# Kernel tuning notes

Hardware: AMD Instinct MI355X
Metric: run time of the kernel (lower is better)

## Reference

```python
import jax, jax.numpy as jnp
import numpy as np

B, C, H, W, HEADS = 8, 192, 128, 128, 4
EPS = 1e-5  # nn.LayerNorm default eps


def conv_block(x, pw_w, pw_b, dw_w, dw_b):
    # pointwise 1x1 conv (C->C) followed by depthwise 3x3 conv (Restormer-style convBlock)
    x = jnp.einsum('bchw,oc->bohw', x, pw_w) + pw_b[None, :, None, None]
    x = jax.lax.conv_general_dilated(
        x, dw_w, window_strides=(1, 1), padding='SAME',
        dimension_numbers=('NCHW', 'OIHW', 'NCHW'),
        feature_group_count=x.shape[1]) + dw_b[None, :, None, None]
    return x


def setup_inputs() -> dict:
    key = jax.random.key(0)
    ks = jax.random.split(key, 10)
    def n(k, shape, scale=0.02):
        return jax.random.normal(k, shape, jnp.float32) * scale
    return {
        'x': jax.random.normal(ks[0], (B, C, H, W), jnp.float32),
        'ln_w': jnp.ones((C,), jnp.float32),
        'ln_b': jnp.zeros((C,), jnp.float32),
        'q_pw_w': n(ks[1], (C, C)), 'q_pw_b': jnp.zeros((C,), jnp.float32),
        'q_dw_w': n(ks[2], (C, 1, 3, 3)), 'q_dw_b': jnp.zeros((C,), jnp.float32),
        'k_pw_w': n(ks[3], (C, C)), 'k_pw_b': jnp.zeros((C,), jnp.float32),
        'k_dw_w': n(ks[4], (C, 1, 3, 3)), 'k_dw_b': jnp.zeros((C,), jnp.float32),
        'v_pw_w': n(ks[5], (C, C)), 'v_pw_b': jnp.zeros((C,), jnp.float32),
        'v_dw_w': n(ks[6], (C, 1, 3, 3)), 'v_dw_b': jnp.zeros((C,), jnp.float32),
        'f_w': n(ks[7], (C, C)), 'f_b': jnp.zeros((C,), jnp.float32),
        'alpha': jnp.ones((), jnp.float32),
    }


def reference(x, ln_w, ln_b, q_pw_w, q_pw_b, q_dw_w, q_dw_b,
              k_pw_w, k_pw_b, k_dw_w, k_dw_b,
              v_pw_w, v_pw_b, v_dw_w, v_dw_b, f_w, f_b, alpha):
    b, c, h, w = x.shape
    s = c // HEADS
    # LayerNorm over channel axis (x.transpose(1,3) -> LN(last dim=C) -> transpose back)
    xt = jnp.transpose(x, (0, 3, 2, 1))  # (B,W,H,C)
    mu = jnp.mean(xt, axis=-1, keepdims=True)
    var = jnp.var(xt, axis=-1, keepdims=True)
    xt = (xt - mu) * jax.lax.rsqrt(var + EPS) * ln_w + ln_b
    xn = jnp.transpose(xt, (0, 3, 2, 1))  # (B,C,H,W) - normalized; residual uses this

    def flat(t):
        # NCHW -> (B, W*H, C), W-major flatten as in the torch code (transpose(1,3) then reshape)
        return jnp.transpose(t, (0, 3, 2, 1)).reshape(b, w * h, c)

    Q = flat(conv_block(xn, q_pw_w, q_pw_b, q_dw_w, q_dw_b))
    K = flat(conv_block(xn, k_pw_w, k_pw_b, k_dw_w, k_dw_b))
    V = flat(conv_block(xn, v_pw_w, v_pw_b, v_dw_w, v_dw_b))

    def heads(t):
        return jnp.transpose(t.reshape(b, w * h, HEADS, s), (0, 2, 1, 3))  # (B,heads,t,s)

    Qh, Kh, Vh = heads(Q), heads(K), heads(V)
    # channel-wise cross-covariance attention: (s x s) per head, learnable temperature alpha
    att = jax.nn.softmax(jnp.einsum('bhts,bhtq->bhsq', Kh, Qh) / alpha, axis=-1)
    out = jnp.einsum('bhts,bhsq->bhtq', Vh, att)  # (B,heads,t,s)
    # view(b,heads,t,s).transpose(2,3).reshape(b, C, H, W) exactly as in torch
    out = jnp.transpose(out, (0, 1, 3, 2)).reshape(b, c, h, w)
    y = jnp.einsum('bchw,oc->bohw', out, f_w) + f_b[None, :, None, None] + xn
    return y
```

## Files before the change

### kernel.cpp

```cpp
#include <hip/hip_runtime.h>
#include <hip/hip_bf16.h>

#define B_    8
#define C_    192
#define H_    128
#define W_    128
#define HW_   16384
#define HEADS 4
#define S_    48
#define EPS_  1e-5f

typedef __hip_bfloat16 bf16;
typedef unsigned short u16;
typedef __attribute__((ext_vector_type(8))) short short8;
typedef __attribute__((ext_vector_type(4))) short short4v;
typedef __attribute__((ext_vector_type(4))) float f32x4;
typedef __attribute__((ext_vector_type(8))) u16 u16x8;
typedef __attribute__((ext_vector_type(4))) u16 u16x4;
typedef __attribute__((ext_vector_type(2))) u16 u16x2;

__device__ inline float ld(const bf16* p)  { return __bfloat162float(*p); }
__device__ inline void  st(float* p, float v) { *p = v; }
__device__ inline void  st(bf16* p, float v)  { *p = __float2bfloat16(v); }
__device__ inline float b2f(u16 u) {
  unsigned v = (unsigned)u << 16;
  return __builtin_bit_cast(float, v);
}
__device__ inline u16 f2b(float f) {
  return __builtin_bit_cast(u16, __float2bfloat16(f));
}

__global__ __launch_bounds__(256) void zero_kernel(float* p, int n) {
  int i = blockIdx.x * 256 + threadIdx.x;
  if (i < n) p[i] = 0.f;
}

__global__ __launch_bounds__(256) void ln_kernel(
    const float* __restrict__ x, const float* __restrict__ lw,
    const float* __restrict__ lb, bf16* __restrict__ xn) {
  __shared__ float4 sS[8][32];
  __shared__ float4 sQ[8][32];
  int tid = threadIdx.x;
  int g = tid >> 5, q = tid & 31;
  int blk = blockIdx.x;
  int b = blk >> 7;
  int pos = (blk & 127) * 128 + q * 4;
  const float* xp = x + (size_t)b * C_ * HW_ + pos;

  float4 v[24];
  float s0 = 0.f, s1 = 0.f, s2 = 0.f, s3 = 0.f;
  float q0 = 0.f, q1 = 0.f, q2 = 0.f, q3 = 0.f;
#pragma unroll
  for (int cc = 0; cc < 24; cc++) {
    int c = g * 24 + cc;
    v[cc] = *(const float4*)&xp[(size_t)c * HW_];
    s0 += v[cc].x; s1 += v[cc].y; s2 += v[cc].z; s3 += v[cc].w;
    q0 += v[cc].x * v[cc].x; q1 += v[cc].y * v[cc].y;
    q2 += v[cc].z * v[cc].z; q3 += v[cc].w * v[cc].w;
  }
  sS[g][q] = make_float4(s0, s1, s2, s3);
  sQ[g][q] = make_float4(q0, q1, q2, q3);
  __syncthreads();

  float S[4] = {}, Qs[4] = {};
#pragma unroll
  for (int gg = 0; gg < 8; gg++) {
    float4 a = sS[gg][q];
    float4 bq = sQ[gg][q];
    S[0] += a.x;  S[1] += a.y;  S[2] += a.z;  S[3] += a.w;
    Qs[0] += bq.x; Qs[1] += bq.y; Qs[2] += bq.z; Qs[3] += bq.w;
  }
  float mu[4], r[4];
#pragma unroll
  for (int i = 0; i < 4; i++) {
    mu[i] = S[i] * (1.0f / C_);
    r[i] = rsqrtf(Qs[i] * (1.0f / C_) - mu[i] * mu[i] + EPS_);
  }

  u16* op = (u16*)xn + (size_t)b * C_ * HW_ + pos;
#pragma unroll
  for (int cc = 0; cc < 24; cc++) {
    int c = g * 24 + cc;
    float wv = lw[c], bv = lb[c];
    u16x4 o;
    o.x = f2b((v[cc].x - mu[0]) * r[0] * wv + bv);
    o.y = f2b((v[cc].y - mu[1]) * r[1] * wv + bv);
    o.z = f2b((v[cc].z - mu[2]) * r[2] * wv + bv);
    o.w = f2b((v[cc].w - mu[3]) * r[3] * wv + bv);
    *(u16x4*)&op[(size_t)c * HW_] = o;
  }
}

#define SWR 200
template <bool RES, typename OutT>
__global__ __launch_bounds__(256) void pw_mfma_kernel(
    const bf16* __restrict__ in, const float* __restrict__ wt,
    const float* __restrict__ bias, const bf16* __restrict__ residual,
    OutT* __restrict__ out) {
  __shared__ __align__(16) u16 sW[64 * SWR];
  __shared__ __align__(16) u16 sX[32 * 256];
  int tid = threadIdx.x;
  int posBase = blockIdx.x * 256;
  int oBase = blockIdx.y * 64;
  int b = blockIdx.z;
  int wv = tid >> 6, lane = tid & 63;
  int quad = lane >> 4, l15 = lane & 15;

#pragma unroll
  for (int i = 0; i < 12; i++) {
    int u = (tid + i * 256) * 4;
    int r = u / 192, c = u % 192;
    float4 f = *(const float4*)&wt[(size_t)(oBase + r) * 192 + c];
    ushort4 hv;
    hv.x = f2b(f.x); hv.y = f2b(f.y); hv.z = f2b(f.z); hv.w = f2b(f.w);
    *(ushort4*)&sW[r * SWR + c] = hv;
  }

  int chl = tid >> 3;
  int oct0 = tid & 7;
  int swz = ((chl >> 3) & 3) << 1;
  const u16* xrow = (const u16*)in + ((size_t)b * C_ + chl) * HW_ + posBase;

  u16x8 vg[4];
#pragma unroll
  for (int i = 0; i < 4; i++)
    vg[i] = *(const u16x8*)&xrow[(oct0 + 8 * i) * 8];

  f32x4 acc[4][4] = {};

  for (int kc = 0; kc < 6; kc++) {
#pragma unroll
    for (int i = 0; i < 4; i++) {
      int s = (oct0 + 8 * i) ^ swz;
      *(u16x8*)&sX[chl * 256 + s * 8] = vg[i];
    }
    __syncthreads();

    if (kc < 5) {
#pragma unroll
      for (int i = 0; i < 4; i++)
        vg[i] = *(const u16x8*)&xrow[(size_t)(kc + 1) * 32 * HW_ + (oct0 + 8 * i) * 8];
    }

    short8 afrag[4];
#pragma unroll
    for (int mt = 0; mt < 4; mt++)
      afrag[mt] = *(const short8*)&sW[(mt * 16 + l15) * SWR + kc * 32 + quad * 8];
#pragma unroll
    for (int nt = 0; nt < 4; nt++) {
      int p = wv * 64 + nt * 16 + l15;
      int po = p >> 3, pr = p & 7;
      int sb = po ^ (quad << 1);
      const u16* bp = &sX[(quad * 8) * 256 + sb * 8 + pr];
      short8 bfrag;
#pragma unroll
      for (int j = 0; j < 8; j++)
        bfrag[j] = (short)bp[j * 256];
#pragma unroll
      for (int mt = 0; mt < 4; mt++)
        acc[mt][nt] = __builtin_amdgcn_mfma_f32_16x16x32_bf16(
            afrag[mt], bfrag, acc[mt][nt], 0, 0, 0);
    }
    __syncthreads();
  }

#pragma unroll
  for (int mt = 0; mt < 4; mt++) {
#pragma unroll
    for (int r = 0; r < 4; r++) {
      int o = oBase + mt * 16 + quad * 4 + r;
      float bs = bias[o];
      size_t rowoff = ((size_t)b * C_ + o) * HW_;
#pragma unroll
      for (int nt = 0; nt < 4; nt++) {
        int p = posBase + wv * 64 + nt * 16 + l15;
        float val = acc[mt][nt][r] + bs;
        if (RES) val += ld(residual + rowoff + p);
        st(out + rowoff + p, val);
      }
    }
  }
}

__global__ __launch_bounds__(256) void dw_kernel(
    const bf16* __restrict__ in, const float* __restrict__ w9,
    const float* __restrict__ bias, bf16* __restrict__ out) {
  __shared__ __align__(16) u16 sT[18 * 128];
  int blk = blockIdx.x;
  int bc = blk >> 3;
  int h0 = (blk & 7) * 16;
  int c = bc % C_;
  const u16* ip = (const u16*)in + (size_t)bc * HW_;
  int tid = threadIdx.x;

  for (int ch = tid; ch < 288; ch += 256) {
    int r = ch >> 4, g = ch & 15;
    int gh = h0 - 1 + r;
    u16x8 val = {};
    if (gh >= 0 && gh < H_) val = *(const u16x8*)&ip[gh * 128 + g * 8];
    *(u16x8*)&sT[r * 128 + g * 8] = val;
  }
  __syncthreads();

  int r_o = tid >> 4, g = tid & 15;
  const float* wp = w9 + c * 9;
  float acc[8];
#pragma unroll
  for (int j = 0; j < 8; j++) acc[j] = bias[c];
#pragma unroll
  for (int k = 0; k < 3; k++) {
    int rr = r_o + k;
    u16x8 mid = *(const u16x8*)&sT[rr * 128 + g * 8];
    float m[8];
#pragma unroll
    for (int j = 0; j < 8; j++) m[j] = b2f(mid[j]);
    float lv = g ? b2f(sT[rr * 128 + g * 8 - 1]) : 0.f;
    float rv = (g < 15) ? b2f(sT[rr * 128 + g * 8 + 8]) : 0.f;
    float wl = wp[k * 3], wc = wp[k * 3 + 1], wr = wp[k * 3 + 2];
#pragma unroll
    for (int j = 0; j < 8; j++) {
      float left  = (j == 0) ? lv : m[j - 1];
      float right = (j == 7) ? rv : m[j + 1];
      acc[j] += wl * left + wc * m[j] + wr * right;
    }
  }
  u16x8 o;
#pragma unroll
  for (int j = 0; j < 8; j++) o[j] = f2b(acc[j]);
  *(u16x8*)((u16*)out + (size_t)bc * HW_ + (h0 + r_o) * 128 + g * 8) = o;
}

__global__ __launch_bounds__(256) void dwt_kernel(
    const bf16* __restrict__ in, const float* __restrict__ w9,
    const float* __restrict__ bias, bf16* __restrict__ out) {
  __shared__ __align__(16) u16 sIn[130 * 32];
  int blk = blockIdx.x;
  int bc = blk >> 3;
  int w0 = (blk & 7) * 16;
  int c = bc % C_;
  const u16* ip = (const u16*)in + (size_t)bc * HW_;
  int tid = threadIdx.x;

  for (int idx = tid; idx < 520; idx += 256) {
    int r = idx >> 2, seg = idx & 3;
    int h = r - 1;
    int w = w0 - 8 + seg * 8;
    u16x8 val = {};
    if (h >= 0 && h < H_ && w >= 0 && w < W_)
      val = *(const u16x8*)&ip[h * W_ + w];
    int colp = (seg * 8) ^ (((r >> 3) & 3) << 4);
    *(u16x8*)&sIn[r * 32 + colp] = val;
  }
  __syncthreads();

  int wl = tid & 15, ho = tid >> 4;
  const float* wp = w9 + c * 9;
  float wk[9];
#pragma unroll
  for (int i = 0; i < 9; i++) wk[i] = wp[i];
  float bs = bias[c];
  float acc[8];
#pragma unroll
  for (int j = 0; j < 8; j++) acc[j] = bs;
#pragma unroll
  for (int k = 0; k < 10; k++) {
    int r = ho * 8 + k;
    int swz = ((r >> 3) & 3) << 4;
    float lv = b2f(sIn[r * 32 + ((wl + 7) ^ swz)]);
    float mv = b2f(sIn[r * 32 + ((wl + 8) ^ swz)]);
    float rv = b2f(sIn[r * 32 + ((wl + 9) ^ swz)]);
#pragma unroll
    for (int kh = 0; kh < 3; kh++) {
      int j = k - kh;
      if (j >= 0 && j < 8)
        acc[j] += wk[kh * 3] * lv + wk[kh * 3 + 1] * mv + wk[kh * 3 + 2] * rv;
    }
  }
  u16x8 o;
#pragma unroll
  for (int j = 0; j < 8; j++) o[j] = f2b(acc[j]);
  *(u16x8*)((u16*)out + (size_t)bc * HW_ + (w0 + wl) * H_ + ho * 8) = o;
}

__global__ __launch_bounds__(256) void gram_mfma_kernel(
    const bf16* __restrict__ Q, const bf16* __restrict__ K,
    float* __restrict__ logits) {
  __shared__ float sP[4][S_ * S_];
  int bh = blockIdx.y;
  int b = bh >> 2, hd = bh & 3;
  int tid = threadIdx.x;
  int wv = tid >> 6, lane = tid & 63;
  int quad = lane >> 4, l15 = lane & 15;
  const u16* Qb = (const u16*)Q + ((size_t)b * C_ + hd * S_) * HW_;
  const u16* Kb = (const u16*)K + ((size_t)b * C_ + hd * S_) * HW_;
  int pbase = blockIdx.x * 1024 + wv * 256 + quad * 8;

  f32x4 acc[3][3] = {};
#pragma unroll
  for (int t = 0; t < 8; t++) {
    int p = pbase + t * 32;
    short8 a[3], bb[3];
#pragma unroll
    for (int mi = 0; mi < 3; mi++)
      a[mi] = *(const short8*)&Kb[(size_t)(mi * 16 + l15) * HW_ + p];
#pragma unroll
    for (int ni = 0; ni < 3; ni++)
      bb[ni] = *(const short8*)&Qb[(size_t)(ni * 16 + l15) * HW_ + p];
#pragma unroll
    for (int mi = 0; mi < 3; mi++)
#pragma unroll
      for (int ni = 0; ni < 3; ni++)
        acc[mi][ni] = __builtin_amdgcn_mfma_f32_16x16x32_bf16(
            a[mi], bb[ni], acc[mi][ni], 0, 0, 0);
  }

#pragma unroll
  for (int mi = 0; mi < 3; mi++)
#pragma unroll
    for (int r = 0; r < 4; r++) {
      int sk = mi * 16 + quad * 4 + r;
#pragma unroll
      for (int ni = 0; ni < 3; ni++)
        sP[wv][sk * S_ + ni * 16 + l15] = acc[mi][ni][r];
    }
  __syncthreads();

  float* lp = logits + (size_t)bh * S_ * S_;
  for (int e = tid; e < S_ * S_; e += 256)
    atomicAdd(&lp[e], sP[0][e] + sP[1][e] + sP[2][e] + sP[3][e]);
}

__global__ __launch_bounds__(256) void softmax_kernel(
    const float* __restrict__ logits, const float* __restrict__ alpha,
    float* __restrict__ att) {
  int row = blockIdx.x * 256 + threadIdx.x;
  if (row >= B_ * HEADS * S_) return;
  float inv_a = 1.0f / alpha[0];
  const float* lp = logits + (size_t)row * S_;
  float v[S_];
  float m = -1e30f;
  for (int i = 0; i < S_; i++) {
    v[i] = lp[i] * inv_a;
    m = fmaxf(m, v[i]);
  }
  float s = 0.f;
  for (int i = 0; i < S_; i++) { v[i] = expf(v[i] - m); s += v[i]; }
  float inv_s = 1.0f / s;
  float* ap = att + (size_t)row * S_;
  for (int i = 0; i < S_; i++) ap[i] = v[i] * inv_s;
}

#define AVP 264
#define ATP 72
__global__ __launch_bounds__(256) void av_mfma_kernel(
    const bf16* __restrict__ V, const float* __restrict__ att,
    bf16* __restrict__ out) {
  __shared__ __align__(16) u16 sV[64 * AVP];
  __shared__ __align__(16) u16 sA[48 * ATP];
  int bh = blockIdx.y;
  int b = bh >> 2, hd = bh & 3;
  int p0 = blockIdx.x * 256;
  int tid = threadIdx.x;
  int wv = tid >> 6, lane = tid & 63;
  int quad = lane >> 4, l15 = lane & 15;
  const u16* Vb = (const u16*)V + ((size_t)b * C_ + hd * S_) * HW_ + p0;
  const float* ap = att + (size_t)bh * S_ * S_;

#pragma unroll
  for (int i = 0; i < 6; i++) {
    int e = tid + i * 256;
    int s = e >> 5, p8 = (e & 31) * 8;
    u16x8 v8 = *(const u16x8*)&Vb[(size_t)s * HW_ + p8];
    *(u16x8*)&sV[s * AVP + p8] = v8;
  }
  {
    unsigned* zp = (unsigned*)&sV[48 * AVP];
    for (int e = tid; e < 16 * AVP / 2; e += 256) zp[e] = 0;
  }
  for (int e = tid; e < S_ * S_; e += 256) {
    int q = e % S_, s = e / S_;
    sA[q * ATP + s] = f2b(ap[e]);
  }
  for (int e = tid; e < S_ * 16; e += 256) {
    int q = e >> 4, s = 48 + (e & 15);
    sA[q * ATP + s] = 0;
  }
  __syncthreads();

  f32x4 acc[3][4] = {};
#pragma unroll
  for (int kc = 0; kc < 2; kc++) {
    short8 afrag[3];
#pragma unroll
    for (int mt = 0; mt < 3; mt++)
      afrag[mt] = *(const short8*)&sA[(mt * 16 + l15) * ATP + kc * 32 + quad * 8];
#pragma unroll
    for (int nt = 0; nt < 4; nt++) {
      int p = wv * 64 + nt * 16 + l15;
      short8 bfrag;
#pragma unroll
      for (int j = 0; j < 8; j++)
        bfrag[j] = (short)sV[(kc * 32 + quad * 8 + j) * AVP + p];
#pragma unroll
      for (int mt = 0; mt < 3; mt++)
        acc[mt][nt] = __builtin_amdgcn_mfma_f32_16x16x32_bf16(
            afrag[mt], bfrag, acc[mt][nt], 0, 0, 0);
    }
  }

  bf16* ob = out + ((size_t)b * C_ + hd * S_) * HW_ + p0;
#pragma unroll
  for (int mt = 0; mt < 3; mt++)
#pragma unroll
    for (int r = 0; r < 4; r++) {
      int q = mt * 16 + quad * 4 + r;
#pragma unroll
      for (int nt = 0; nt < 4; nt++) {
        int p = wv * 64 + nt * 16 + l15;
        st(ob + (size_t)q * HW_ + p, acc[mt][nt][r]);
      }
    }
}

extern "C" void kernel_launch(void* const* d_in, const int* in_sizes, int n_in,
                              void* d_out, int out_size, void* d_ws, size_t ws_size,
                              hipStream_t stream) {
  const float* x      = (const float*)d_in[0];
  const float* ln_w   = (const float*)d_in[1];
  const float* ln_b   = (const float*)d_in[2];
  const float* q_pw_w = (const float*)d_in[3];
  const float* q_pw_b = (const float*)d_in[4];
  const float* q_dw_w = (const float*)d_in[5];
  const float* q_dw_b = (const float*)d_in[6];
  const float* k_pw_w = (const float*)d_in[7];
  const float* k_pw_b = (const float*)d_in[8];
  const float* k_dw_w = (const float*)d_in[9];
  const float* k_dw_b = (const float*)d_in[10];
  const float* v_pw_w = (const float*)d_in[11];
  const float* v_pw_b = (const float*)d_in[12];
  const float* v_dw_w = (const float*)d_in[13];
  const float* v_dw_b = (const float*)d_in[14];
  const float* f_w    = (const float*)d_in[15];
  const float* f_b    = (const float*)d_in[16];
  const float* alpha  = (const float*)d_in[17];
  float* out = (float*)d_out;

  size_t N = (size_t)B_ * C_ * HW_;
  bf16* xn   = (bf16*)d_ws;
  bf16* tmp  = xn + N;
  bf16* A    = tmp + N;
  float* logits = (float*)(A + N);
  float* att    = logits + (size_t)B_ * HEADS * S_ * S_;
  bf16* Kb     = (bf16*)d_out;

  int nlog = B_ * HEADS * S_ * S_;
  zero_kernel<<<dim3(nlog / 256), 256, 0, stream>>>(logits, nlog);

  ln_kernel<<<dim3(B_ * HW_ / 128), 256, 0, stream>>>(x, ln_w, ln_b, xn);

  dim3 gG(HW_ / 256, C_ / 64, B_);
  int dwBlocks = B_ * C_ * 8;

  pw_mfma_kernel<false, bf16><<<gG, 256, 0, stream>>>(xn, q_pw_w, q_pw_b, nullptr, tmp);
  dw_kernel<<<dwBlocks, 256, 0, stream>>>(tmp, q_dw_w, q_dw_b, A);
  pw_mfma_kernel<false, bf16><<<gG, 256, 0, stream>>>(xn, k_pw_w, k_pw_b, nullptr, tmp);
  dw_kernel<<<dwBlocks, 256, 0, stream>>>(tmp, k_dw_w, k_dw_b, Kb);
  gram_mfma_kernel<<<dim3(16, B_ * HEADS), 256, 0, stream>>>(A, Kb, logits);
  softmax_kernel<<<dim3(6), 256, 0, stream>>>(logits, alpha, att);
  pw_mfma_kernel<false, bf16><<<gG, 256, 0, stream>>>(xn, v_pw_w, v_pw_b, nullptr, tmp);
  dwt_kernel<<<dwBlocks, 256, 0, stream>>>(tmp, v_dw_w, v_dw_b, A);
  av_mfma_kernel<<<dim3(HW_ / 256, B_ * HEADS), 256, 0, stream>>>(A, att, tmp);
  pw_mfma_kernel<true, float><<<gG, 256, 0, stream>>>(tmp, f_w, f_b, xn, out);
}
```

Baseline: 458.5 us.

## Store LN and attention outputs in MFMA-fragment-tiled layout, drop LDS staging in pointwise GEMM

Result: faster. 447.3 us (-2.4%).

```diff
diff --git a/kernel.cpp b/kernel.cpp
--- a/kernel.cpp
+++ b/kernel.cpp
@@ -19,6 +19,7 @@
 typedef __attribute__((ext_vector_type(4))) u16 u16x4;
 typedef __attribute__((ext_vector_type(2))) u16 u16x2;
 
+
 __device__ inline float ld(const bf16* p)  { return __bfloat162float(*p); }
 __device__ inline void  st(float* p, float v) { *p = v; }
 __device__ inline void  st(bf16* p, float v)  { *p = __float2bfloat16(v); }
@@ -47,17 +48,19 @@
   int pos = (blk & 127) * 128 + q * 4;
   const float* xp = x + (size_t)b * C_ * HW_ + pos;
 
-  float4 v[24];
+  float4 v[3][8];
   float s0 = 0.f, s1 = 0.f, s2 = 0.f, s3 = 0.f;
   float q0 = 0.f, q1 = 0.f, q2 = 0.f, q3 = 0.f;
 #pragma unroll
-  for (int cc = 0; cc < 24; cc++) {
-    int c = g * 24 + cc;
-    v[cc] = *(const float4*)&xp[(size_t)c * HW_];
-    s0 += v[cc].x; s1 += v[cc].y; s2 += v[cc].z; s3 += v[cc].w;
-    q0 += v[cc].x * v[cc].x; q1 += v[cc].y * v[cc].y;
-    q2 += v[cc].z * v[cc].z; q3 += v[cc].w * v[cc].w;
-  }
+  for (int t = 0; t < 3; t++)
+#pragma unroll
+    for (int ci = 0; ci < 8; ci++) {
+      int c = t * 64 + g * 8 + ci;
+      float4 f = *(const float4*)&xp[(size_t)c * HW_];
+      v[t][ci] = f;
+      s0 += f.x; s1 += f.y; s2 += f.z; s3 += f.w;
+      q0 += f.x * f.x; q1 += f.y * f.y; q2 += f.z * f.z; q3 += f.w * f.w;
+    }
   sS[g][q] = make_float4(s0, s1, s2, s3);
   sQ[g][q] = make_float4(q0, q1, q2, q3);
   __syncthreads();
@@ -77,17 +80,22 @@
     r[i] = rsqrtf(Qs[i] * (1.0f / C_) - mu[i] * mu[i] + EPS_);
   }
 
-  u16* op = (u16*)xn + (size_t)b * C_ * HW_ + pos;
-#pragma unroll
-  for (int cc = 0; cc < 24; cc++) {
-    int c = g * 24 + cc;
-    float wv = lw[c], bv = lb[c];
-    u16x4 o;
-    o.x = f2b((v[cc].x - mu[0]) * r[0] * wv + bv);
-    o.y = f2b((v[cc].y - mu[1]) * r[1] * wv + bv);
-    o.z = f2b((v[cc].z - mu[2]) * r[2] * wv + bv);
-    o.w = f2b((v[cc].w - mu[3]) * r[3] * wv + bv);
-    *(u16x4*)&op[(size_t)c * HW_] = o;
+  u16* base = (u16*)xn + (size_t)b * C_ * HW_ +
+              (size_t)((blk & 127) * 8 + (q >> 2)) * 3072;
+#pragma unroll
+  for (int t = 0; t < 3; t++) {
+#pragma unroll
+    for (int j = 0; j < 4; j++) {
+      u16x8 o8;
+#pragma unroll
+      for (int ci = 0; ci < 8; ci++) {
+        int c = t * 64 + g * 8 + ci;
+        float xv = (j == 0) ? v[t][ci].x : (j == 1) ? v[t][ci].y
+                 : (j == 2) ? v[t][ci].z : v[t][ci].w;
+        o8[ci] = f2b((xv - mu[j]) * r[j] * lw[c] + lb[c]);
+      }
+      *(u16x8*)&base[(t * 8 + g) * 128 + ((q & 3) * 4 + j) * 8] = o8;
+    }
   }
 }
 
@@ -98,7 +106,6 @@
     const float* __restrict__ bias, const bf16* __restrict__ residual,
     OutT* __restrict__ out) {
   __shared__ __align__(16) u16 sW[64 * SWR];
-  __shared__ __align__(16) u16 sX[32 * 256];
   int tid = threadIdx.x;
   int posBase = blockIdx.x * 256;
   int oBase = blockIdx.y * 64;
@@ -109,61 +116,48 @@
 #pragma unroll
   for (int i = 0; i < 12; i++) {
     int u = (tid + i * 256) * 4;
-    int r = u / 192, c = u % 192;
-    float4 f = *(const float4*)&wt[(size_t)(oBase + r) * 192 + c];
+    int rr = u / 192, cc = u % 192;
+    float4 f = *(const float4*)&wt[(size_t)(oBase + rr) * 192 + cc];
     ushort4 hv;
     hv.x = f2b(f.x); hv.y = f2b(f.y); hv.z = f2b(f.z); hv.w = f2b(f.w);
-    *(ushort4*)&sW[r * SWR + c] = hv;
-  }
-
-  int chl = tid >> 3;
-  int oct0 = tid & 7;
-  int swz = ((chl >> 3) & 3) << 1;
-  const u16* xrow = (const u16*)in + ((size_t)b * C_ + chl) * HW_ + posBase;
-
-  u16x8 vg[4];
-#pragma unroll
-  for (int i = 0; i < 4; i++)
-    vg[i] = *(const u16x8*)&xrow[(oct0 + 8 * i) * 8];
+    *(ushort4*)&sW[rr * SWR + cc] = hv;
+  }
+
+  const u16* xb = (const u16*)in + (size_t)b * C_ * HW_ +
+                  (size_t)((posBase >> 4) + wv * 4) * 3072 + quad * 128 + l15 * 8;
+
+  short8 bf[2][4];
+#pragma unroll
+  for (int nt = 0; nt < 4; nt++)
+    bf[0][nt] = *(const short8*)&xb[nt * 3072];
+
+  __syncthreads();
 
   f32x4 acc[4][4] = {};
-
+#pragma unroll
   for (int kc = 0; kc < 6; kc++) {
-#pragma unroll
-    for (int i = 0; i < 4; i++) {
-      int s = (oct0 + 8 * i) ^ swz;
-      *(u16x8*)&sX[chl * 256 + s * 8] = vg[i];
-    }
-    __syncthreads();
-
     if (kc < 5) {
 #pragma unroll
-      for (int i = 0; i < 4; i++)
-        vg[i] = *(const u16x8*)&xrow[(size_t)(kc + 1) * 32 * HW_ + (oct0 + 8 * i) * 8];
-    }
-
+      for (int nt = 0; nt < 4; nt++)
+        bf[(kc + 1) & 1][nt] =
+            *(const short8*)&xb[nt * 3072 + (kc + 1) * 512];
+    }
     short8 afrag[4];
 #pragma unroll
     for (int mt = 0; mt < 4; mt++)
       afrag[mt] = *(const short8*)&sW[(mt * 16 + l15) * SWR + kc * 32 + quad * 8];
 #pragma unroll
-    for (int nt = 0; nt < 4; nt++) {
-      int p = wv * 64 + nt * 16 + l15;
-      int po = p >> 3, pr = p & 7;
-      int sb = po ^ (quad << 1);
-      const u16* bp = &sX[(quad * 8) * 256 + sb * 8 + pr];
-      short8 bfrag;
-#pragma unroll
-      for (int j = 0; j < 8; j++)
-        bfrag[j] = (short)bp[j * 256];
+    for (int nt = 0; nt < 4; nt++)
 #pragma unroll
       for (int mt = 0; mt < 4; mt++)
         acc[mt][nt] = __builtin_amdgcn_mfma_f32_16x16x32_bf16(
-            afrag[mt], bfrag, acc[mt][nt], 0, 0, 0);
-    }
-    __syncthreads();
-  }
-
+            afrag[mt], bf[kc & 1][nt], acc[mt][nt], 0, 0, 0);
+  }
+
+  const u16* rb = nullptr;
+  if (RES)
+    rb = (const u16*)residual + (size_t)b * C_ * HW_ +
+         (size_t)((posBase >> 4) + wv * 4) * 3072 + l15 * 8;
 #pragma unroll
   for (int mt = 0; mt < 4; mt++) {
 #pragma unroll
@@ -175,7 +169,7 @@
       for (int nt = 0; nt < 4; nt++) {
         int p = posBase + wv * 64 + nt * 16 + l15;
         float val = acc[mt][nt][r] + bs;
-        if (RES) val += ld(residual + rowoff + p);
+        if (RES) val += b2f(rb[nt * 3072 + (o >> 3) * 128 + (o & 7)]);
         st(out + rowoff + p, val);
       }
     }
@@ -408,17 +402,17 @@
     }
   }
 
-  bf16* ob = out + ((size_t)b * C_ + hd * S_) * HW_ + p0;
+  u16* ob = (u16*)out + (size_t)b * C_ * HW_ + (size_t)(p0 >> 4) * 3072;
 #pragma unroll
   for (int mt = 0; mt < 3; mt++)
 #pragma unroll
     for (int r = 0; r < 4; r++) {
-      int q = mt * 16 + quad * 4 + r;
-#pragma unroll
-      for (int nt = 0; nt < 4; nt++) {
-        int p = wv * 64 + nt * 16 + l15;
-        st(ob + (size_t)q * HW_ + p, acc[mt][nt][r]);
-      }
+      int ql = mt * 16 + quad * 4 + r;
+      int ch = hd * S_ + ql;
+      int cb = (ch >> 3) * 128 + (ch & 7);
+#pragma unroll
+      for (int nt = 0; nt < 4; nt++)
+        ob[(size_t)(wv * 4 + nt) * 3072 + cb + l15 * 8] = f2b(acc[mt][nt][r]);
     }
 }
 
```
